# Performance work log

Hardware: AMD Instinct MI355X
Metric: run time of the kernel (lower is better)

Reference implementation:

```python
import jax, jax.numpy as jnp
import numpy as np

SEGMENT_LENGTHS = [1024, 2048, 4096]
DILATION_RATES = [1, 2, 4]


def setup_inputs() -> dict:
    key = jax.random.key(0)
    k1, k2, k3 = jax.random.split(key, 3)
    n = sum(SEGMENT_LENGTHS)  # 7168
    shape = (1, n, 8, 64)  # (b, n, h, d)
    q = jax.random.normal(k1, shape, dtype=jnp.float32)
    k = jax.random.normal(k2, shape, dtype=jnp.float32)
    v = jax.random.normal(k3, shape, dtype=jnp.float32)
    return {"q": q, "k": k, "v": v}


def _attend(q_seg, k_kv, v_kv):
    # q_seg: [b, q_len, h, d]; k_kv/v_kv: [b, k_len, h, d]
    d = q_seg.shape[-1]
    scale = 1.0 / jnp.sqrt(jnp.asarray(d, q_seg.dtype))
    scores = jnp.einsum("bqhd,bkhd->bhqk", q_seg, k_kv) * scale
    w = jax.nn.softmax(scores, axis=-1)
    return jnp.einsum("bhqk,bkhd->bqhd", w, v_kv)


def reference(q, k, v):
    # Single-device dilated attention (ring_size == 1, is_causal=False).
    n = q.shape[1]
    output = jnp.zeros_like(q)
    seg_start = 0
    for seg_len, dilation in zip(SEGMENT_LENGTHS, DILATION_RATES):
        if seg_start >= n:
            break
        seg_end = min(seg_start + seg_len, n)
        q_seg = q[:, seg_start:seg_end]
        if dilation > 1:
            k_d = k[:, ::dilation]
            v_d = v[:, ::dilation]
        else:
            k_d, v_d = k, v
        out_seg = _attend(q_seg, k_d, v_d)
        output = output.at[:, seg_start:seg_end].set(out_seg)
        seg_start = seg_end
    return output
```

## Files before the change

kernel.cpp:

```cpp
#include <hip/hip_runtime.h>

#define VB0 3670016L
#define VB1 7340032L
#define VB2 9175040L
#define PO_OFF 5046272L

typedef short bvec8 __attribute__((ext_vector_type(8)));
typedef float fvec16 __attribute__((ext_vector_type(16)));
typedef _Float16 hvec4 __attribute__((ext_vector_type(4)));
typedef _Float16 hvec8 __attribute__((ext_vector_type(8)));

#if defined(__has_builtin)
#if __has_builtin(__builtin_amdgcn_cvt_pk_bf16_f32)
#define HAVE_CVTPK 1
#endif
#if __has_builtin(__builtin_amdgcn_permlane32_swap)
#define HAVE_PLSWAP 1
#endif
#endif

static __device__ __forceinline__ unsigned pk2(float a, float b) {
#ifdef HAVE_CVTPK
  auto r = __builtin_amdgcn_cvt_pk_bf16_f32(a, b);
  unsigned u; __builtin_memcpy(&u, &r, 4);
  return u;
#else
  unsigned ua = (__float_as_uint(a) + 0x8000u) >> 16;
  unsigned ub = (__float_as_uint(b) + 0x8000u) & 0xffff0000u;
  return ua | ub;
#endif
}
static __device__ __forceinline__ void async16(const short* g, short* l) {
  __builtin_amdgcn_global_load_lds((const __attribute__((address_space(1))) unsigned*)(void*)g,
                                   (__attribute__((address_space(3))) unsigned*)(void*)l, 16, 0, 0);
}

__global__ __launch_bounds__(256) void pack_all(const float* __restrict__ k,
                                                const float* __restrict__ v,
                                                short* __restrict__ W) {
  __shared__ float tl[64][65];
  int b = blockIdx.x, t = threadIdx.x;
  if (b < 896) {
    int h = b / 112, tile = b % 112, i0 = tile * 64;
    int r = t >> 2, c = t & 3;
    const float* src = k + ((long)(i0 + r) * 8 + h) * 64 + c * 16;
    short* dst = W + ((long)h * 7168 + i0 + r) * 64 + c * 16;
    union { unsigned u[8]; bvec8 v[2]; } tw;
#pragma unroll
    for (int q4 = 0; q4 < 4; q4++) {
      float4 x = *(const float4*)(src + q4 * 4);
      tw.u[q4 * 2 + 0] = pk2(x.x, x.y);
      tw.u[q4 * 2 + 1] = pk2(x.z, x.w);
    }
    *(bvec8*)dst = tw.v[0];
    *(bvec8*)(dst + 8) = tw.v[1];
  } else {
    int b2 = b - 896;
    int h, tile, dil, L; long base;
    if (b2 < 896)       { L = 7168; dil = 1; h = b2 / 112; tile = b2 % 112; base = VB0; }
    else if (b2 < 1344) { int bb = b2 - 896;  L = 3584; dil = 2; h = bb / 56; tile = bb % 56; base = VB1; }
    else                { int bb = b2 - 1344; L = 1792; dil = 4; h = bb / 28; tile = bb % 28; base = VB2; }
    int i0 = tile * 64;
    int row = t >> 2, c = t & 3;
    const float* src = v + ((long)(i0 + row) * dil * 8 + h) * 64;
#pragma unroll
    for (int cc = 0; cc < 4; cc++) {
      int d0 = c * 16 + cc * 4;
      float4 x = *(const float4*)(src + d0);
      tl[row][d0 + 0] = x.x; tl[row][d0 + 1] = x.y;
      tl[row][d0 + 2] = x.z; tl[row][d0 + 3] = x.w;
    }
    __syncthreads();
    int d = t >> 2, part = t & 3;
    union { unsigned u[8]; bvec8 v[2]; } tw;
#pragma unroll
    for (int u2 = 0; u2 < 8; u2++)
      tw.u[u2] = pk2(tl[part * 16 + 2 * u2][d], tl[part * 16 + 2 * u2 + 1][d]);
    short* dst = W + base + ((long)h * 64 + d) * L + i0 + part * 16;
    *(bvec8*)dst = tw.v[0];
    *(bvec8*)(dst + 8) = tw.v[1];
  }
}

#ifdef HAVE_PLSWAP
#define PEXCH(fu, da0, da1, db0, db1)                                              \
  do {                                                                             \
    auto rr0 = __builtin_amdgcn_permlane32_swap((int)(da0), (int)(db0), false, false); \
    auto rr1 = __builtin_amdgcn_permlane32_swap((int)(da1), (int)(db1), false, false); \
    __builtin_memcpy(&fu.u4[0], &rr0, 4);                                          \
    __builtin_memcpy(&fu.u4[2], (const char*)&rr0 + 4, 4);                         \
    __builtin_memcpy(&fu.u4[1], &rr1, 4);                                          \
    __builtin_memcpy(&fu.u4[3], (const char*)&rr1 + 4, 4);                         \
  } while (0)
#else
#define PEXCH(fu, da0, da1, db0, db1)                                              \
  do {                                                                             \
    unsigned s0 = hb ? (da0) : (db0), s1 = hb ? (da1) : (db1);                     \
    unsigned x0 = __shfl_xor(s0, 32), x1 = __shfl_xor(s1, 32);                     \
    fu.u4[0] = hb ? x0 : (da0);  fu.u4[1] = hb ? x1 : (da1);                       \
    fu.u4[2] = hb ? (db0) : x0;  fu.u4[3] = hb ? (db1) : x1;                       \
  } while (0)
#endif

#define SOFTMAX_PV_H(SA, V0, V1, SP)                                               \
  do {                                                                             \
    const int r0_ = (SP) * 8;                                                      \
    float p[8];                                                                    \
    _Pragma("unroll") for (int u = 0; u < 8; u++)                                  \
        p[u] = __builtin_amdgcn_exp2f(SA[r0_ + u]);                                \
    lacc += ((p[0] + p[1]) + (p[2] + p[3])) + ((p[4] + p[5]) + (p[6] + p[7]));     \
    unsigned da0 = pk2(p[0], p[1]), da1 = pk2(p[2], p[3]);                         \
    unsigned db0 = pk2(p[4], p[5]), db1 = pk2(p[6], p[7]);                         \
    union { unsigned u4[4]; bvec8 v; } fu;                                         \
    PEXCH(fu, da0, da1, db0, db1);                                                 \
    __builtin_amdgcn_s_setprio(1);                                                 \
    Oa[0] = __builtin_amdgcn_mfma_f32_32x32x16_bf16((V0), fu.v, Oa[0], 0, 0, 0);   \
    Oa[1] = __builtin_amdgcn_mfma_f32_32x32x16_bf16((V1), fu.v, Oa[1], 0, 0, 0);   \
    __builtin_amdgcn_s_setprio(0);                                                 \
  } while (0)

__global__ __launch_bounds__(256, 4) void attn_kern(const float* __restrict__ q,
                                                    const short* __restrict__ W,
                                                    float* __restrict__ out,
                                                    _Float16* __restrict__ POh,
                                                    _Float16* __restrict__ PLh) {
  int b = blockIdx.x;
  int h, q0, dil, kt0, L, NT, pb; long vbo;
  if (b < 256) {
    h = b & 7; int qt = b >> 3;
    q0 = 3072 + qt * 128; dil = 4; L = 1792; vbo = VB2; kt0 = 0; NT = 28; pb = -1;
  } else if (b < 768) {
    int i = b - 256; int sp = i & 7; h = (i >> 3) & 7; int qt = i >> 6;
    q0 = qt * 128; dil = 1; L = 7168; vbo = VB0; kt0 = sp * 14; NT = 14; pb = i;
  } else {
    int i = b - 768; int sp = i & 3; h = (i >> 2) & 7; int qt = i >> 5;
    q0 = 1024 + qt * 128; dil = 2; L = 3584; vbo = VB1; kt0 = sp * 14; NT = 14; pb = 512 + i;
  }
  const short* kb = W + (long)h * 7168 * 64;
  const short* vt = W + vbo + (long)h * 64 * L;
  const int dil64 = dil * 64;

  __shared__ __attribute__((aligned(16))) short sK[2][4096];
  __shared__ __attribute__((aligned(16))) short sV[2][4096];
  short* sKf = &sK[0][0];
  short* sVf = &sV[0][0];

  int t = threadIdx.x, lane = t & 63, w = t >> 6;
  int ln = lane & 31, hb = lane >> 5;

  bvec8 qb[4];
  {
    const float* qp = q + ((long)(q0 + w * 32 + ln) * 8 + h) * 64 + 8 * hb;
    const float qs = 0.125f * 1.44269504088896f;
#pragma unroll
    for (int ks = 0; ks < 4; ks++) {
      union { unsigned u[4]; bvec8 v; } qu;
#pragma unroll
      for (int jj = 0; jj < 4; jj++)
        qu.u[jj] = pk2(qs * qp[ks * 16 + 2 * jj], qs * qp[ks * 16 + 2 * jj + 1]);
      qb[ks] = qu.v;
    }
  }

  int srow = lane >> 3, sch = (lane & 7) ^ srow;
  const long kstep = 64L * dil64;
  const short* gk0; const short* gk1; const short* gv0; const short* gv1;
  {
    int row0 = (w * 2 + 0) * 8 + srow, row1 = (w * 2 + 1) * 8 + srow;
    long kb0 = (long)kt0 * 64;
    gk0 = kb + (kb0 + row0) * dil64 + sch * 8;
    gk1 = kb + (kb0 + row1) * dil64 + sch * 8;
    gv0 = vt + (long)row0 * L + kb0 + sch * 8;
    gv1 = vt + (long)row1 * L + kb0 + sch * 8;
  }
  const int ldoff = w * 2 * 512;
  auto stage = [&](int bo2) {
    async16(gk0, sKf + bo2 + ldoff);
    async16(gv0, sVf + bo2 + ldoff);
    async16(gk1, sKf + bo2 + ldoff + 512);
    async16(gv1, sVf + bo2 + ldoff + 512);
    gk0 += kstep; gk1 += kstep; gv0 += 64; gv1 += 64;
  };

  stage(0);

  int koff[8];
#pragma unroll
  for (int ks = 0; ks < 4; ks++)
#pragma unroll
    for (int mb = 0; mb < 2; mb++)
      koff[ks * 2 + mb] = (mb * 32 + ln) * 64 + (((2 * ks + hb) ^ (ln & 7)) * 8);

  fvec16 Oa[2];
  float lacc = 0.f;
#pragma unroll
  for (int i = 0; i < 16; i++) { Oa[0][i] = 0.f; Oa[1][i] = 0.f; }

  int bo = 0;
  for (int it = 0; it < NT; it++) {
    __syncthreads();
    if (it < NT - 1) stage(bo ^ 4096);

    const short* sb = sKf + bo;
    const short* vb = sVf + bo;
    bo ^= 4096;

#pragma unroll
    for (int half = 0; half < 2; half++) {
      fvec16 Sa;
#pragma unroll
      for (int i = 0; i < 16; i++) Sa[i] = 0.f;
      __builtin_amdgcn_s_setprio(1);
#pragma unroll
      for (int ks = 0; ks < 4; ks++) {
        bvec8 kf = *(const bvec8*)(sb + koff[ks * 2 + half]);
        Sa = __builtin_amdgcn_mfma_f32_32x32x16_bf16(kf, qb[ks], Sa, 0, 0, 0);
      }
      __builtin_amdgcn_s_setprio(0);

      bvec8 v00 = *(const bvec8*)(vb + koff[(2 * half) * 2 + 0]);
      bvec8 v01 = *(const bvec8*)(vb + koff[(2 * half) * 2 + 1]);
      bvec8 v10 = *(const bvec8*)(vb + koff[(2 * half + 1) * 2 + 0]);
      bvec8 v11 = *(const bvec8*)(vb + koff[(2 * half + 1) * 2 + 1]);

      SOFTMAX_PV_H(Sa, v00, v01, 0);
      SOFTMAX_PV_H(Sa, v10, v11, 1);
    }
  }

  float lf = lacc + __shfl_xor(lacc, 32);
  int wl = w * 32 + ln;
  if (pb >= 0) {
    _Float16* po = POh + ((long)pb * 128 + wl) * 64;
#pragma unroll
    for (int mb2 = 0; mb2 < 2; mb2++)
#pragma unroll
      for (int r2 = 0; r2 < 4; r2++) {
        hvec4 x = { (_Float16)Oa[mb2][r2 * 4 + 0], (_Float16)Oa[mb2][r2 * 4 + 1],
                    (_Float16)Oa[mb2][r2 * 4 + 2], (_Float16)Oa[mb2][r2 * 4 + 3] };
        *(hvec4*)(po + mb2 * 32 + r2 * 8 + hb * 4) = x;
      }
    if (hb == 0) PLh[(long)pb * 128 + wl] = (_Float16)lf;
  } else {
    float inv = 1.f / lf;
    float* op = out + ((long)(q0 + wl) * 8 + h) * 64;
#pragma unroll
    for (int mb2 = 0; mb2 < 2; mb2++)
#pragma unroll
      for (int r2 = 0; r2 < 4; r2++) {
        float4 x = { Oa[mb2][r2 * 4 + 0] * inv, Oa[mb2][r2 * 4 + 1] * inv,
                     Oa[mb2][r2 * 4 + 2] * inv, Oa[mb2][r2 * 4 + 3] * inv };
        *(float4*)(op + mb2 * 32 + r2 * 8 + hb * 4) = x;
      }
  }
}

__global__ __launch_bounds__(256) void combine_kern(const _Float16* __restrict__ POh,
                                                    const _Float16* __restrict__ PLh,
                                                    float* __restrict__ out) {
  int g = blockIdx.x, t = threadIdx.x;
  int base, nsp, q0, h;
  if (g < 64) { int qt = g >> 3; h = g & 7; base = qt * 64 + h * 8; nsp = 8; q0 = qt * 128; }
  else { int gi = g - 64; int qt = gi >> 3; h = gi & 7; base = 512 + qt * 32 + h * 4; nsp = 4; q0 = 1024 + qt * 128; }
  int r = t >> 1, ch = (t & 1) * 32;
  float lt = 0.f;
  for (int sp = 0; sp < nsp; sp++) lt += (float)PLh[(long)(base + sp) * 128 + r];
  float inv = 1.f / lt;
  float acc[32];
#pragma unroll
  for (int j = 0; j < 32; j++) acc[j] = 0.f;
  for (int sp = 0; sp < nsp; sp++) {
    const hvec8* pb8 = (const hvec8*)(POh + ((long)(base + sp) * 128 + r) * 64 + ch);
#pragma unroll
    for (int j = 0; j < 4; j++) {
      hvec8 x = pb8[j];
#pragma unroll
      for (int kk = 0; kk < 8; kk++) acc[j * 8 + kk] += (float)x[kk];
    }
  }
  float4* op = (float4*)(out + ((long)(q0 + r) * 8 + h) * 64 + ch);
#pragma unroll
  for (int j = 0; j < 8; j++) {
    float4 x = { acc[j * 4 + 0] * inv, acc[j * 4 + 1] * inv,
                 acc[j * 4 + 2] * inv, acc[j * 4 + 3] * inv };
    op[j] = x;
  }
}

extern "C" void kernel_launch(void* const* d_in, const int* in_sizes, int n_in,
                              void* d_out, int out_size, void* d_ws, size_t ws_size,
                              hipStream_t stream) {
  const float* q = (const float*)d_in[0];
  const float* k = (const float*)d_in[1];
  const float* v = (const float*)d_in[2];
  float* out = (float*)d_out;
  short* W = (short*)d_ws;
  _Float16* POh = (_Float16*)((float*)d_ws + PO_OFF);
  _Float16* PLh = POh + 1024L * 128 * 64;

  pack_all<<<2464, 256, 0, stream>>>(k, v, W);
  attn_kern<<<1280, 256, 0, stream>>>(q, W, out, POh, PLh);
  combine_kern<<<192, 256, 0, stream>>>(POh, PLh, out);
}
```

Measured before the change: 158.8 us.

## Load K/V tiles straight into registers, dropping LDS staging and barriers

The attention loop no longer stages K and V tiles into double-buffered shared memory with async global-to-LDS copies and per-tile __syncthreads. Each wave now loads its MFMA operand fragments for K and V directly from global memory into registers, prefetching the next tile's fragments while the current tile's QK and PV MFMAs run. Launch bounds drop from 4 to 3 blocks per CU to leave room for the extra fragment registers. This removes LDS traffic and block-level synchronisation, but every wave now fetches the full K/V tile on its own, which multiplies L1/L2 traffic by the wave count. Global loads are strided by row, and the final prefetch reads past the last tile.

```diff
diff --git a/kernel.cpp b/kernel.cpp
--- a/kernel.cpp
+++ b/kernel.cpp
@@ -29,10 +29,6 @@
   unsigned ub = (__float_as_uint(b) + 0x8000u) & 0xffff0000u;
   return ua | ub;
 #endif
-}
-static __device__ __forceinline__ void async16(const short* g, short* l) {
-  __builtin_amdgcn_global_load_lds((const __attribute__((address_space(1))) unsigned*)(void*)g,
-                                   (__attribute__((address_space(3))) unsigned*)(void*)l, 16, 0, 0);
 }
 
 __global__ __launch_bounds__(256) void pack_all(const float* __restrict__ k,
@@ -119,7 +115,7 @@
     __builtin_amdgcn_s_setprio(0);                                                 \
   } while (0)
 
-__global__ __launch_bounds__(256, 4) void attn_kern(const float* __restrict__ q,
+__global__ __launch_bounds__(256, 3) void attn_kern(const float* __restrict__ q,
                                                     const short* __restrict__ W,
                                                     float* __restrict__ out,
                                                     _Float16* __restrict__ POh,
@@ -140,11 +136,6 @@
   const short* vt = W + vbo + (long)h * 64 * L;
   const int dil64 = dil * 64;
 
-  __shared__ __attribute__((aligned(16))) short sK[2][4096];
-  __shared__ __attribute__((aligned(16))) short sV[2][4096];
-  short* sKf = &sK[0][0];
-  short* sVf = &sV[0][0];
-
   int t = threadIdx.x, lane = t & 63, w = t >> 6;
   int ln = lane & 31, hb = lane >> 5;
 
@@ -162,70 +153,60 @@
     }
   }
 
-  int srow = lane >> 3, sch = (lane & 7) ^ srow;
   const long kstep = 64L * dil64;
-  const short* gk0; const short* gk1; const short* gv0; const short* gv1;
-  {
-    int row0 = (w * 2 + 0) * 8 + srow, row1 = (w * 2 + 1) * 8 + srow;
-    long kb0 = (long)kt0 * 64;
-    gk0 = kb + (kb0 + row0) * dil64 + sch * 8;
-    gk1 = kb + (kb0 + row1) * dil64 + sch * 8;
-    gv0 = vt + (long)row0 * L + kb0 + sch * 8;
-    gv1 = vt + (long)row1 * L + kb0 + sch * 8;
-  }
-  const int ldoff = w * 2 * 512;
-  auto stage = [&](int bo2) {
-    async16(gk0, sKf + bo2 + ldoff);
-    async16(gv0, sVf + bo2 + ldoff);
-    async16(gk1, sKf + bo2 + ldoff + 512);
-    async16(gv1, sVf + bo2 + ldoff + 512);
-    gk0 += kstep; gk1 += kstep; gv0 += 64; gv1 += 64;
-  };
-
-  stage(0);
-
-  int koff[8];
-#pragma unroll
-  for (int ks = 0; ks < 4; ks++)
-#pragma unroll
-    for (int mb = 0; mb < 2; mb++)
-      koff[ks * 2 + mb] = (mb * 32 + ln) * 64 + (((2 * ks + hb) ^ (ln & 7)) * 8);
+  const short* kp0 = kb + (long)kt0 * kstep;
+  const short* kp1 = kp0 + 32 * dil64;
+  const short* vp  = vt + kt0 * 64;
+  const int lk  = ln * dil64 + hb * 8;
+  const int lv0 = ln * L + hb * 8;
+  const int lv1 = (32 + ln) * L + hb * 8;
+
+  bvec8 kf[8], vf[8];
+#pragma unroll
+  for (int ks = 0; ks < 4; ks++) {
+    kf[ks]     = *(const bvec8*)(kp0 + lk + ks * 16);
+    kf[4 + ks] = *(const bvec8*)(kp1 + lk + ks * 16);
+  }
+#pragma unroll
+  for (int s = 0; s < 4; s++) {
+    vf[s * 2 + 0] = *(const bvec8*)(vp + lv0 + s * 16);
+    vf[s * 2 + 1] = *(const bvec8*)(vp + lv1 + s * 16);
+  }
+  kp0 += kstep; kp1 += kstep; vp += 64;
 
   fvec16 Oa[2];
   float lacc = 0.f;
 #pragma unroll
   for (int i = 0; i < 16; i++) { Oa[0][i] = 0.f; Oa[1][i] = 0.f; }
 
-  int bo = 0;
   for (int it = 0; it < NT; it++) {
-    __syncthreads();
-    if (it < NT - 1) stage(bo ^ 4096);
-
-    const short* sb = sKf + bo;
-    const short* vb = sVf + bo;
-    bo ^= 4096;
-
 #pragma unroll
     for (int half = 0; half < 2; half++) {
+      const short* kp = half ? kp1 : kp0;
       fvec16 Sa;
 #pragma unroll
       for (int i = 0; i < 16; i++) Sa[i] = 0.f;
       __builtin_amdgcn_s_setprio(1);
 #pragma unroll
-      for (int ks = 0; ks < 4; ks++) {
-        bvec8 kf = *(const bvec8*)(sb + koff[ks * 2 + half]);
-        Sa = __builtin_amdgcn_mfma_f32_32x32x16_bf16(kf, qb[ks], Sa, 0, 0, 0);
+      for (int ks = 0; ks < 4; ks++)
+        Sa = __builtin_amdgcn_mfma_f32_32x32x16_bf16(kf[half * 4 + ks], qb[ks], Sa, 0, 0, 0);
+      __builtin_amdgcn_s_setprio(0);
+
+#pragma unroll
+      for (int ks = 0; ks < 4; ks++)
+        kf[half * 4 + ks] = *(const bvec8*)(kp + lk + ks * 16);
+
+      SOFTMAX_PV_H(Sa, vf[half * 4 + 0], vf[half * 4 + 1], 0);
+      SOFTMAX_PV_H(Sa, vf[half * 4 + 2], vf[half * 4 + 3], 1);
+
+#pragma unroll
+      for (int s2 = 0; s2 < 2; s2++) {
+        int s = half * 2 + s2;
+        vf[half * 4 + s2 * 2 + 0] = *(const bvec8*)(vp + lv0 + s * 16);
+        vf[half * 4 + s2 * 2 + 1] = *(const bvec8*)(vp + lv1 + s * 16);
       }
-      __builtin_amdgcn_s_setprio(0);
-
-      bvec8 v00 = *(const bvec8*)(vb + koff[(2 * half) * 2 + 0]);
-      bvec8 v01 = *(const bvec8*)(vb + koff[(2 * half) * 2 + 1]);
-      bvec8 v10 = *(const bvec8*)(vb + koff[(2 * half + 1) * 2 + 0]);
-      bvec8 v11 = *(const bvec8*)(vb + koff[(2 * half + 1) * 2 + 1]);
-
-      SOFTMAX_PV_H(Sa, v00, v01, 0);
-      SOFTMAX_PV_H(Sa, v10, v11, 1);
-    }
+    }
+    kp0 += kstep; kp1 += kstep; vp += 64;
   }
 
   float lf = lacc + __shfl_xor(lacc, 32);
```

After: 261.4 us. 1.65x slower.
